# Performance work log

Hardware: AMD Instinct MI355X
Metric: run time of the kernel (lower is better)

Reference implementation:

```python
import jax, jax.numpy as jnp
import numpy as np

# Param packing order: [capacitance_x, capacitance_y] + for each direction in
# (ax, by, xy, yx, xx, yy): [conductance, mean, std, pot]  -> total 26 scalars.
_DIR = {"ax": 0, "by": 1, "xy": 2, "yx": 3, "xx": 4, "yy": 5}

B, T = 4096, 4096


def setup_inputs() -> dict:
    key = jax.random.key(0)
    inputs = jax.random.normal(key, (B, T, 2), dtype=jnp.float32)
    # initializer constants from the keras layer
    params = jnp.asarray([1.0, 1.0] + [0.001, 0.3, 3.0, 1.0] * 6, dtype=jnp.float32)
    return {"inputs": inputs, "params": params}


def reference(inputs, params):
    cap_x, cap_y = params[0], params[1]

    def syn(d, pre, post):
        i = 2 + 4 * _DIR[d]
        g, mean, std, pot = params[i], params[i + 1], params[i + 2], params[i + 3]
        return g * jax.nn.sigmoid(std * (pre - mean)) * (pot - post)

    def step(state, inp):
        x, y = state                      # each [B, 1]
        a, b = inp[:, :1], inp[:, 1:]     # each [B, 1]
        cur_x = syn("ax", a, x) + syn("yx", y, x) + syn("xx", x, x)
        cur_y = syn("by", b, y) + syn("xy", x, y) + syn("yy", y, y)
        x = x + cur_x / cap_x
        y = y + cur_y / cap_y
        out = jnp.concatenate((x, y), axis=-1)  # [B, 2]
        return (x, y), out

    bsz = inputs.shape[0]
    x0 = jnp.zeros((bsz, 1), inputs.dtype)
    y0 = jnp.ones((bsz, 1), inputs.dtype)   # initial state = concat(zeros, ones)
    _, outs = jax.lax.scan(step, (x0, y0), jnp.swapaxes(inputs, 0, 1))  # [T, B, 2]
    return jnp.swapaxes(outs, 0, 1)  # [B, T, 2]
```

## Files before the change

### kernel.cpp

```cpp
#include <hip/hip_runtime.h>

#define TLEN  4096
#define NROWS 4096
#define RPB   32
#define K     32
#define NC    (TLEN / K)
#define LDPAD 66
#define SGSL  (16 * 32)
#define STSL  (RPB * LDPAD)
#define UN    8

__device__ __forceinline__ float fexp2(float x) { return __builtin_amdgcn_exp2f(x); }
__device__ __forceinline__ float frcp(float x)  { return __builtin_amdgcn_rcpf(x); }
__device__ __forceinline__ float sigz(float z)  { return frcp(1.0f + fexp2(z)); }

__device__ __forceinline__ float lane_swap1(float v) {
    int r = __builtin_amdgcn_update_dpp(0, __float_as_int(v), 0xB1, 0xF, 0xF, true);
    return __int_as_float(r);
}

__device__ void run_fast(const float* __restrict__ inp, const float* __restrict__ prm,
                         float* __restrict__ out,
                         float4* __restrict__ sgbuf,
                         float*  __restrict__ st) {
    const int tid  = threadIdx.x;
    const int wid  = tid >> 6;
    const int lane = tid & 63;
    const int R0   = blockIdx.x * RPB;
    const float L2E = 1.4426950408889634f;
    float2* __restrict__ out2 = (float2*)out;

    if (wid == 1) {
        const int r = lane & 31, h = lane >> 5;
        const float c1x = -prm[4] * L2E, c0x = prm[4] * prm[3] * L2E;
        const float c1y = -prm[8] * L2E, c0y = prm[8] * prm[7] * L2E;
        const float4* __restrict__ src = (const float4*)inp + (size_t)(R0 + r) * (TLEN / 2);

        float4 bufA[8], bufB[8];

        auto produce_reg = [&](const float4* buf, int c) {
            float4* sl = sgbuf + ((c & 1) ? SGSL : 0);
#pragma unroll
            for (int j = 0; j < 8; ++j) {
                float4 v = buf[j];
                float4 o;
                o.x = sigz(__builtin_fmaf(c1x, v.x, c0x));
                o.y = sigz(__builtin_fmaf(c1y, v.y, c0y));
                o.z = sigz(__builtin_fmaf(c1x, v.z, c0x));
                o.w = sigz(__builtin_fmaf(c1y, v.w, c0y));
                sl[(h * 8 + j) * 32 + r] = o;
            }
        };
        auto flush = [&](int c) {
            const float* sl = st + ((c & 1) ? STSL : 0);
            const int col = lane & 31;
#pragma unroll
            for (int j = 0; j < 16; ++j) {
                int ro = 2 * j + (lane >> 5);
                float2 v = *(const float2*)&sl[ro * LDPAD + col * 2];
                out2[(size_t)(R0 + ro) * TLEN + (size_t)c * K + col] = v;
            }
        };

#pragma unroll
        for (int j = 0; j < 8; ++j) bufA[j] = src[h * 8 + j];
        produce_reg(bufA, 0);
#pragma unroll
        for (int j = 0; j < 8; ++j) bufB[j] = src[16 + h * 8 + j];
        __syncthreads();
        for (int c = 0; c < NC; ++c) {
            if ((c & 1) == 0) {
                if (c + 1 < NC) produce_reg(bufB, c + 1);
                if (c + 2 < NC) {
#pragma unroll
                    for (int j = 0; j < 8; ++j)
                        bufA[j] = src[(c + 2) * 16 + h * 8 + j];
                }
            } else {
                if (c + 1 < NC) produce_reg(bufA, c + 1);
                if (c + 2 < NC) {
#pragma unroll
                    for (int j = 0; j < 8; ++j)
                        bufB[j] = src[(c + 2) * 16 + h * 8 + j];
                }
            }
            if (c >= 1) flush(c - 1);
            __syncthreads();
        }
        flush(NC - 1);
    } else {
        const int r_  = lane >> 1;
        const int par = lane & 1;
        const int inB = par ? 6 : 2, sfB = par ? 22 : 18, t2B = par ? 10 : 14;
        const float ic  = 1.0f / prm[par];
        const float g1  = prm[sfB] * ic, P1 = g1 * prm[sfB + 3], Gn1 = -g1;
        const float g2  = prm[t2B] * ic, P2 = g2 * prm[t2B + 3], Gn2 = -g2;
        const float gA  = prm[inB] * ic, PA = gA * prm[inB + 3], GnA = -gA;
        const float sdz = prm[sfB + 2];
        const float c1s = -sdz * L2E, c0s = sdz * prm[sfB + 1] * L2E;

        float x   = par ? 1.0f : 0.0f;
        float sig = sigz(__builtin_fmaf(c1s, x, c0s));
        float u   = __builtin_fmaf(-sig, sig, sig);

        auto resync = [&]() {
            sig = sigz(__builtin_fmaf(c1s, x, c0s));
            u   = __builtin_fmaf(-sig, sig, sig);
        };

        auto step = [&](float sg, float* wp, int t) {
            float Av  = __builtin_fmaf(GnA, x, PA);
            float t1v = __builtin_fmaf(Gn1, x, P1);
            float t2v = __builtin_fmaf(Gn2, x, P2);
            float m   = sg * Av;
            float b2  = __builtin_fmaf(sig, t1v, m);
            float sc  = lane_swap1(sig);
            float dx  = __builtin_fmaf(sc, t2v, b2);
            x = x + dx;
            wp[2 * t] = x;
            float dz = sdz * dx;
            sig = __builtin_fmaf(u, dz, sig);
            u   = __builtin_fmaf(-sig, sig, sig);
        };

        __syncthreads();
        for (int c = 0; c < NC; ++c) {
            const float4* lb = sgbuf + ((c & 1) ? SGSL : 0);
            float* wp = st + ((c & 1) ? STSL : 0) + r_ * LDPAD + par;
            float4 f0 = lb[r_];
            float4 f1 = lb[32 + r_];
#pragma unroll
            for (int tp = 0; tp < 16; ++tp) {
                float4 f = f0; f0 = f1;
                if (tp < 14) f1 = lb[(tp + 2) * 32 + r_];
                step(par ? f.y : f.x, wp, 2 * tp);
                step(par ? f.w : f.z, wp, 2 * tp + 1);
                if (tp == 7) resync();
            }
            resync();
            __syncthreads();
        }
    }
}

struct LaneConst {
    float c1_in, c0_in, c1_sf, c0_sf, c1_ot, c0_ot;
    float gS_in, gS_cr, gS_sf, gP_in, gP_cr, gP_sf;
};

__device__ __forceinline__ float do_step_exact(float s, float pre_in, const LaneConst& k) {
    float sig_in = sigz(__builtin_fmaf(k.c1_in, pre_in, k.c0_in));
    float sig_sf = sigz(__builtin_fmaf(k.c1_sf, s, k.c0_sf));
    float sig_ot = sigz(__builtin_fmaf(k.c1_ot, s, k.c0_ot));
    float sig_cr = lane_swap1(sig_ot);
    float S = __builtin_fmaf(k.gS_in, sig_in, __builtin_fmaf(k.gS_cr, sig_cr, k.gS_sf * sig_sf));
    float P = __builtin_fmaf(k.gP_in, sig_in, __builtin_fmaf(k.gP_cr, sig_cr, k.gP_sf * sig_sf));
    return s + __builtin_fmaf(S, -s, P);
}

__device__ void run_exact(const float* __restrict__ inp, const float* __restrict__ prm,
                          float* __restrict__ out) {
    const int tid = blockIdx.x * 128 + threadIdx.x;
    const int row = tid >> 1;
    if (row >= NROWS) return;
    const int par = tid & 1;
    const float L2E = 1.4426950408889634f;
    const int inB = par ? 6 : 2, sfB = par ? 22 : 18, otB = par ? 14 : 10, crB = par ? 10 : 14;
    const float invc = 1.0f / prm[par];
    LaneConst k;
    float sd = prm[inB + 2], mn = prm[inB + 1];
    k.c1_in = -sd * L2E; k.c0_in = sd * mn * L2E;
    sd = prm[sfB + 2]; mn = prm[sfB + 1];
    k.c1_sf = -sd * L2E; k.c0_sf = sd * mn * L2E;
    sd = prm[otB + 2]; mn = prm[otB + 1];
    k.c1_ot = -sd * L2E; k.c0_ot = sd * mn * L2E;
    k.gS_in = prm[inB] * invc; k.gP_in = k.gS_in * prm[inB + 3];
    k.gS_sf = prm[sfB] * invc; k.gP_sf = k.gS_sf * prm[sfB + 3];
    k.gS_cr = prm[crB] * invc; k.gP_cr = k.gS_cr * prm[crB + 3];

    const float4* __restrict__ src = (const float4*)inp + (size_t)row * (TLEN / 2);
    float* __restrict__ dst = out + (size_t)row * (TLEN * 2) + par;
    float s = par ? 1.0f : 0.0f;

    float4 cur[UN], nxt[UN];
#pragma unroll
    for (int j = 0; j < UN; ++j) cur[j] = src[j];
    const int NIT = TLEN / (2 * UN);
    for (int it = 0; it < NIT; ++it) {
        if (it + 1 < NIT) {
#pragma unroll
            for (int j = 0; j < UN; ++j) nxt[j] = src[(it + 1) * UN + j];
        }
        float* dptr = dst + it * (UN * 4);
#pragma unroll
        for (int j = 0; j < UN; ++j) {
            float4 f = cur[j];
            s = do_step_exact(s, par ? f.y : f.x, k);
            dptr[j * 4] = s;
            s = do_step_exact(s, par ? f.w : f.z, k);
            dptr[j * 4 + 2] = s;
        }
#pragma unroll
        for (int j = 0; j < UN; ++j) cur[j] = nxt[j];
    }
}

__global__ __launch_bounds__(128, 1)
void memcell_scan(const float* __restrict__ inp, const float* __restrict__ prm,
                  float* __restrict__ out) {
    __shared__ float4 sgbuf[2 * SGSL];
    __shared__ float  st[2 * STSL];

    const bool shared = (prm[11] == prm[19]) && (prm[12] == prm[20]) &&
                        (prm[15] == prm[23]) && (prm[16] == prm[24]);
    const float capx = prm[0], capy = prm[1];
    const bool gpos = prm[2] >= 0.f && prm[6] >= 0.f && prm[10] >= 0.f &&
                      prm[14] >= 0.f && prm[18] >= 0.f && prm[22] >= 0.f &&
                      capx > 0.f && capy > 0.f;
    const float sx = (prm[2] + prm[14] + prm[18]) / capx;
    const float sy = (prm[6] + prm[10] + prm[22]) / capy;
    const float lox = fminf(0.f, fminf(prm[5], fminf(prm[17], prm[21])));
    const float hix = fmaxf(0.f, fmaxf(prm[5], fmaxf(prm[17], prm[21])));
    const float loy = fminf(1.f, fminf(prm[9], fminf(prm[13], prm[25])));
    const float hiy = fmaxf(1.f, fmaxf(prm[9], fmaxf(prm[13], prm[25])));
    const float wbx = prm[20] * sx * (hix - lox), wby = prm[24] * sy * (hiy - loy);
    const float zmx = prm[20] * fmaxf(fabsf(lox - prm[19]), fabsf(hix - prm[19]));
    const float zmy = prm[24] * fmaxf(fabsf(loy - prm[23]), fabsf(hiy - prm[23]));
    const bool fast = shared && gpos && sx <= 0.25f && sy <= 0.25f &&
                      wbx <= 0.02f && wby <= 0.02f && zmx <= 20.f && zmy <= 20.f;
    if (fast) {
        run_fast(inp, prm, out, sgbuf, st);
    } else {
        run_exact(inp, prm, out);
    }
}

extern "C" void kernel_launch(void* const* d_in, const int* in_sizes, int n_in,
                              void* d_out, int out_size, void* d_ws, size_t ws_size,
                              hipStream_t stream) {
    (void)in_sizes; (void)n_in; (void)d_ws; (void)ws_size; (void)out_size;
    const float* inp = (const float*)d_in[0];
    const float* prm = (const float*)d_in[1];
    float* out = (float*)d_out;
    memcell_scan<<<dim3(NROWS / RPB), dim3(128), 0, stream>>>(inp, prm, out);
}
```

Baseline: 341.3 us.

## Precompute input-synapse coefficients in producer wave and pack scan stores

The producer wave now pre-multiplies the input sigmoid by the scaled conductance and reversal terms, so the serial scan forms the input current with a single FMA. Each lane reads only its own direction's slice, and the u update runs once per two steps instead of every step. Results are written as float2 pairs per lane into a per-lane transposed staging layout, and the flush is changed to match. The aim is a shorter dependent chain in the recurrence, at the cost of twice the LDS sigmoid buffer and a small accuracy change from the stale u in the linearised sigmoid update.

```diff
diff --git a/kernel.cpp b/kernel.cpp
--- a/kernel.cpp
+++ b/kernel.cpp
@@ -5,9 +5,10 @@
 #define RPB   32
 #define K     32
 #define NC    (TLEN / K)
-#define LDPAD 66
-#define SGSL  (16 * 32)
-#define STSL  (RPB * LDPAD)
+#define SGSL  (2 * 16 * 32)
+#define DIRS  (16 * 32)
+#define STP   34
+#define STSL  (64 * STP)
 #define UN    8
 
 __device__ __forceinline__ float fexp2(float x) { return __builtin_amdgcn_exp2f(x); }
@@ -34,21 +35,29 @@
         const int r = lane & 31, h = lane >> 5;
         const float c1x = -prm[4] * L2E, c0x = prm[4] * prm[3] * L2E;
         const float c1y = -prm[8] * L2E, c0y = prm[8] * prm[7] * L2E;
+        const float gAx = prm[2] / prm[0], PAx = gAx * prm[5], GnAx = -gAx;
+        const float gAy = prm[6] / prm[1], PAy = gAy * prm[9], GnAy = -gAy;
         const float4* __restrict__ src = (const float4*)inp + (size_t)(R0 + r) * (TLEN / 2);
 
         float4 bufA[8], bufB[8];
 
         auto produce_reg = [&](const float4* buf, int c) {
-            float4* sl = sgbuf + ((c & 1) ? SGSL : 0);
+            float4* slX = sgbuf + ((c & 1) ? SGSL : 0);
+            float4* slY = slX + DIRS;
 #pragma unroll
             for (int j = 0; j < 8; ++j) {
+                const int tp = h * 8 + j;
                 float4 v = buf[j];
-                float4 o;
-                o.x = sigz(__builtin_fmaf(c1x, v.x, c0x));
-                o.y = sigz(__builtin_fmaf(c1y, v.y, c0y));
-                o.z = sigz(__builtin_fmaf(c1x, v.z, c0x));
-                o.w = sigz(__builtin_fmaf(c1y, v.w, c0y));
-                sl[(h * 8 + j) * 32 + r] = o;
+                float sx0 = sigz(__builtin_fmaf(c1x, v.x, c0x));
+                float sy0 = sigz(__builtin_fmaf(c1y, v.y, c0y));
+                float sx1 = sigz(__builtin_fmaf(c1x, v.z, c0x));
+                float sy1 = sigz(__builtin_fmaf(c1y, v.w, c0y));
+                float4 ox; ox.x = GnAx * sx0; ox.y = PAx * sx0;
+                           ox.z = GnAx * sx1; ox.w = PAx * sx1;
+                float4 oy; oy.x = GnAy * sy0; oy.y = PAy * sy0;
+                           oy.z = GnAy * sy1; oy.w = PAy * sy1;
+                slX[tp * 32 + r] = ox;
+                slY[tp * 32 + r] = oy;
             }
         };
         auto flush = [&](int c) {
@@ -57,7 +66,9 @@
 #pragma unroll
             for (int j = 0; j < 16; ++j) {
                 int ro = 2 * j + (lane >> 5);
-                float2 v = *(const float2*)&sl[ro * LDPAD + col * 2];
+                float2 v;
+                v.x = sl[(2 * ro)     * STP + col];
+                v.y = sl[(2 * ro + 1) * STP + col];
                 out2[(size_t)(R0 + ro) * TLEN + (size_t)c * K + col] = v;
             }
         };
@@ -91,11 +102,10 @@
     } else {
         const int r_  = lane >> 1;
         const int par = lane & 1;
-        const int inB = par ? 6 : 2, sfB = par ? 22 : 18, t2B = par ? 10 : 14;
+        const int sfB = par ? 22 : 18, t2B = par ? 10 : 14;
         const float ic  = 1.0f / prm[par];
         const float g1  = prm[sfB] * ic, P1 = g1 * prm[sfB + 3], Gn1 = -g1;
         const float g2  = prm[t2B] * ic, P2 = g2 * prm[t2B + 3], Gn2 = -g2;
-        const float gA  = prm[inB] * ic, PA = gA * prm[inB + 3], GnA = -gA;
         const float sdz = prm[sfB + 2];
         const float c1s = -sdz * L2E, c0s = sdz * prm[sfB + 1] * L2E;
 
@@ -108,33 +118,38 @@
             u   = __builtin_fmaf(-sig, sig, sig);
         };
 
-        auto step = [&](float sg, float* wp, int t) {
-            float Av  = __builtin_fmaf(GnA, x, PA);
-            float t1v = __builtin_fmaf(Gn1, x, P1);
-            float t2v = __builtin_fmaf(Gn2, x, P2);
-            float m   = sg * Av;
-            float b2  = __builtin_fmaf(sig, t1v, m);
-            float sc  = lane_swap1(sig);
-            float dx  = __builtin_fmaf(sc, t2v, b2);
-            x = x + dx;
-            wp[2 * t] = x;
-            float dz = sdz * dx;
-            sig = __builtin_fmaf(u, dz, sig);
-            u   = __builtin_fmaf(-sig, sig, sig);
-        };
-
         __syncthreads();
         for (int c = 0; c < NC; ++c) {
-            const float4* lb = sgbuf + ((c & 1) ? SGSL : 0);
-            float* wp = st + ((c & 1) ? STSL : 0) + r_ * LDPAD + par;
+            const float4* lb = sgbuf + ((c & 1) ? SGSL : 0) + par * DIRS;
+            float* wp = st + ((c & 1) ? STSL : 0) + lane * STP;
             float4 f0 = lb[r_];
             float4 f1 = lb[32 + r_];
 #pragma unroll
             for (int tp = 0; tp < 16; ++tp) {
                 float4 f = f0; f0 = f1;
                 if (tp < 14) f1 = lb[(tp + 2) * 32 + r_];
-                step(par ? f.y : f.x, wp, 2 * tp);
-                step(par ? f.w : f.z, wp, 2 * tp + 1);
+                float m1  = __builtin_fmaf(f.x, x, f.y);
+                float t1v = __builtin_fmaf(Gn1, x, P1);
+                float t2v = __builtin_fmaf(Gn2, x, P2);
+                float b21 = __builtin_fmaf(sig, t1v, m1);
+                float sc1 = lane_swap1(sig);
+                float dxa = __builtin_fmaf(sc1, t2v, b21);
+                x = x + dxa;
+                float xa  = x;
+                float dza = sdz * dxa;
+                sig = __builtin_fmaf(u, dza, sig);
+                float m2   = __builtin_fmaf(f.z, x, f.w);
+                float t1v2 = __builtin_fmaf(Gn1, x, P1);
+                float t2v2 = __builtin_fmaf(Gn2, x, P2);
+                float b22  = __builtin_fmaf(sig, t1v2, m2);
+                float sc2  = lane_swap1(sig);
+                float dxb  = __builtin_fmaf(sc2, t2v2, b22);
+                x = x + dxb;
+                float dzb = sdz * dxb;
+                sig = __builtin_fmaf(u, dzb, sig);
+                u   = __builtin_fmaf(-sig, sig, sig);
+                float2 w2; w2.x = xa; w2.y = x;
+                *(float2*)(wp + 2 * tp) = w2;
                 if (tp == 7) resync();
             }
             resync();
```

Result: slower. 395.6 us (+15.9%).
